# Optimization experiments

Measured on AMD Instinct MI355X. Metric: run time of the kernel, lower is better.

Reference implementation:

```python
import jax, jax.numpy as jnp
import numpy as np

B, L, D, H, DK, DV, DFF = 4, 2048, 1024, 16, 64, 64, 4096
EPS = 1e-6


def setup_inputs() -> dict:
    key = jax.random.key(0)
    ks = jax.random.split(key, 16)
    s = lambda fan_in: 1.0 / np.sqrt(fan_in)
    inp = {
        "src": jax.random.normal(ks[0], (B, L, D), jnp.float32),
        "slf_attn_mask": jax.random.randint(ks[1], (B, L), 0, 2, jnp.int32),
        "prior_weight": jax.random.uniform(ks[2], (B, L, L), jnp.float32),
        # attention params (torch Linear weight layout: [out, in], no bias for qkv/fc)
        "ln1_g": jnp.ones((D,), jnp.float32),
        "ln1_b": jnp.zeros((D,), jnp.float32),
        "wq": jax.random.normal(ks[3], (H * DK, D), jnp.float32) * s(D),
        "wk": jax.random.normal(ks[4], (H * DK, D), jnp.float32) * s(D),
        "wv": jax.random.normal(ks[5], (H * DV, D), jnp.float32) * s(D),
        "fc_w": jax.random.normal(ks[6], (D, H * DV), jnp.float32) * s(H * DV),
        # FFN params
        "ln2_g": jnp.ones((D,), jnp.float32),
        "ln2_b": jnp.zeros((D,), jnp.float32),
        "w1_w": jax.random.normal(ks[7], (DFF, D), jnp.float32) * s(D),
        "w1_b": jnp.zeros((DFF,), jnp.float32),
        "w2_w": jax.random.normal(ks[8], (D, DFF), jnp.float32) * s(DFF),
        "w2_b": jnp.zeros((D,), jnp.float32),
    }
    return inp


def _layer_norm(x, g, b):
    mu = jnp.mean(x, axis=-1, keepdims=True)
    var = jnp.mean(jnp.square(x - mu), axis=-1, keepdims=True)
    return (x - mu) * jax.lax.rsqrt(var + EPS) * g + b


def reference(src, slf_attn_mask, prior_weight, ln1_g, ln1_b, wq, wk, wv, fc_w,
              ln2_g, ln2_b, w1_w, w1_b, w2_w, w2_b):
    b, l, d = src.shape
    # --- multi-head self attention (pre-LN) ---
    x = _layer_norm(src, ln1_g, ln1_b)
    q = (x @ wq.T).reshape(b, l, H, DK).transpose(0, 2, 1, 3)  # [b,h,l,dk]
    k = (x @ wk.T).reshape(b, l, H, DK).transpose(0, 2, 1, 3)
    v = (x @ wv.T).reshape(b, l, H, DV).transpose(0, 2, 1, 3)
    temperature = jnp.asarray(DK, src.dtype) ** 0.5
    attn = jnp.einsum("bhqd,bhkd->bhqk", q / temperature, k)
    attn = attn * prior_weight[:, None]                     # [b,1,q,k] broadcast over heads
    attn = jnp.where(slf_attn_mask[:, None, None, :] == 0, -1e9, attn)  # key padding mask
    attn = jax.nn.softmax(attn, axis=-1)
    o = jnp.einsum("bhqk,bhkd->bhqd", attn, v)
    o = o.transpose(0, 2, 1, 3).reshape(b, l, H * DV)
    y = o @ fc_w.T + src                                     # residual
    # --- position-wise FFN (pre-LN) ---
    z = _layer_norm(y, ln2_g, ln2_b)
    h = jax.nn.relu(z @ w1_w.T + w1_b)
    y = h @ w2_w.T + w2_b + y                                # residual
    return (y, attn)
```

## Files before the change

kernel.cpp:

```cpp
#include <hip/hip_runtime.h>
#include <stdint.h>
#include <stddef.h>

#define BB 4
#define LL 2048
#define DD 1024
#define HH 16
#define DKK 64
#define DFFN 4096

typedef __bf16 bf16;
typedef __attribute__((ext_vector_type(4))) float f32x4;
typedef __attribute__((ext_vector_type(8))) bf16 bf16x8;
typedef __attribute__((ext_vector_type(4))) bf16 bf16x4;

__device__ __forceinline__ void async_ld16(const void* g, void* l) {
  __builtin_amdgcn_global_load_lds(
      (const __attribute__((address_space(1))) void*)g,
      (__attribute__((address_space(3))) void*)l, 16, 0, 0);
}

__global__ __launch_bounds__(256) void cvt_kernel(
    const float* __restrict__ in, bf16* __restrict__ out, int n4) {
  int i = blockIdx.x * 256 + threadIdx.x;
  if (i >= n4) return;
  f32x4 v = ((const f32x4*)in)[i];
  bf16x4 o;
  o[0] = (bf16)v.x; o[1] = (bf16)v.y; o[2] = (bf16)v.z; o[3] = (bf16)v.w;
  ((bf16x4*)out)[i] = o;
}

__global__ __launch_bounds__(256) void ln_kernel(
    const float* __restrict__ x, const float* __restrict__ gam,
    const float* __restrict__ bet, bf16* __restrict__ out) {
  int row = blockIdx.x;
  const float* xr = x + (size_t)row * DD;
  int t = threadIdx.x, wave = t >> 6, lane = t & 63;
  f32x4 v = *(const f32x4*)(xr + (t << 2));
  float s = v.x + v.y + v.z + v.w;
  float q2 = v.x * v.x + v.y * v.y + v.z * v.z + v.w * v.w;
#pragma unroll
  for (int off = 32; off; off >>= 1) {
    s += __shfl_xor(s, off);
    q2 += __shfl_xor(q2, off);
  }
  __shared__ float a1[4], a2[4];
  if (lane == 0) { a1[wave] = s; a2[wave] = q2; }
  __syncthreads();
  s = a1[0] + a1[1] + a1[2] + a1[3];
  q2 = a2[0] + a2[1] + a2[2] + a2[3];
  float mean = s * (1.0f / DD);
  float var = q2 * (1.0f / DD) - mean * mean;
  float rs = rsqrtf(var + 1e-6f);
  f32x4 g = *(const f32x4*)(gam + (t << 2));
  f32x4 b = *(const f32x4*)(bet + (t << 2));
  bf16x4 o;
  o[0] = (bf16)((v.x - mean) * rs * g.x + b.x);
  o[1] = (bf16)((v.y - mean) * rs * g.y + b.y);
  o[2] = (bf16)((v.z - mean) * rs * g.z + b.z);
  o[3] = (bf16)((v.w - mean) * rs * g.w + b.w);
  *(bf16x4*)&out[(size_t)row * DD + (t << 2)] = o;
}

template <int BN, bool AF32, bool OUTF32, bool HASBIAS, bool DORELU,
          bool HASRES, bool PVMODE>
__global__ __launch_bounds__(256, 2) void gemm_bt(
    const void* __restrict__ Ain, const bf16* __restrict__ Bm,
    void* __restrict__ Cout, const float* __restrict__ bias,
    const float* __restrict__ res, int K, int ldc) {
  constexpr int BM = 128, BK = 32;
  constexpr int WN = BN / 32;
  static_assert(BN == 64 || BN == 128, "BN");
  __shared__ bf16 As[BM * BK];
  __shared__ bf16 Bs[BN * BK];
  int tid = threadIdx.x;
  int wave = tid >> 6, lane = tid & 63;
  int quad = lane >> 4, lm = lane & 15;
  int wm = wave & 1, wn = wave >> 1;
  int m0 = blockIdx.x * BM;
  int n0 = PVMODE ? 0 : blockIdx.y * BN;

  const bf16* Ab = (const bf16*)Ain;
  const float* Af = (const float*)Ain;
  size_t c_off = 0;
  if constexpr (PVMODE) {
    int pb = blockIdx.y;
    int ph = blockIdx.z;
    size_t bh = (size_t)(pb * HH + ph);
    Af += bh * (size_t)LL * LL;
    Bm += bh * (size_t)DKK * LL;
    c_off = (size_t)pb * ((size_t)LL * DD) + (size_t)ph * DKK;
  }

  f32x4 acc[4][WN];
#pragma unroll
  for (int i = 0; i < 4; i++)
#pragma unroll
    for (int j = 0; j < WN; j++) acc[i][j] = (f32x4)0.0f;

  for (int k0 = 0; k0 < K; k0 += BK) {
    __syncthreads();
    if constexpr (AF32) {
#pragma unroll
      for (int it = 0; it < 2; ++it) {
        int chunk = tid + it * 256;
        int row = chunk >> 2;
        int kc = (chunk & 3) << 3;
        const float* sp = Af + (size_t)(m0 + row) * K + k0 + kc;
        f32x4 u0 = *(const f32x4*)sp;
        f32x4 u1 = *(const f32x4*)(sp + 4);
        bf16x8 wv;
        wv[0] = (bf16)u0.x; wv[1] = (bf16)u0.y; wv[2] = (bf16)u0.z; wv[3] = (bf16)u0.w;
        wv[4] = (bf16)u1.x; wv[5] = (bf16)u1.y; wv[6] = (bf16)u1.z; wv[7] = (bf16)u1.w;
        *(bf16x8*)&As[chunk << 3] = wv;
      }
    } else {
#pragma unroll
      for (int it = 0; it < 2; ++it) {
        int chunk = it * 256 + (wave << 6) + lane;
        int row = chunk >> 2;
        int kc = (chunk & 3) << 3;
        async_ld16(Ab + (size_t)(m0 + row) * K + k0 + kc, &As[chunk << 3]);
      }
    }
#pragma unroll
    for (int it = 0; it < BN / 64; ++it) {
      int chunk = it * 256 + (wave << 6) + lane;
      int row = chunk >> 2;
      int kc = (chunk & 3) << 3;
      async_ld16(Bm + (size_t)(n0 + row) * K + k0 + kc, &Bs[chunk << 3]);
    }
    __syncthreads();
    bf16x8 af[4], bfr[WN];
#pragma unroll
    for (int i = 0; i < 4; i++)
      af[i] = *(const bf16x8*)&As[(((wm << 6) + (i << 4) + lm) << 5) + (quad << 3)];
#pragma unroll
    for (int j = 0; j < WN; j++)
      bfr[j] = *(const bf16x8*)&Bs[((wn * (BN / 2) + (j << 4) + lm) << 5) + (quad << 3)];
#pragma unroll
    for (int i = 0; i < 4; i++)
#pragma unroll
      for (int j = 0; j < WN; j++)
        acc[i][j] = __builtin_amdgcn_mfma_f32_16x16x32_bf16(af[i], bfr[j], acc[i][j], 0, 0, 0);
  }

  float* Cf = (float*)Cout;
  bf16* Cb = (bf16*)Cout;
#pragma unroll
  for (int i = 0; i < 4; i++) {
    int rowb = m0 + (wm << 6) + (i << 4) + (quad << 2);
#pragma unroll
    for (int r = 0; r < 4; r++) {
      int row = rowb + r;
#pragma unroll
      for (int j = 0; j < WN; j++) {
        int col = n0 + wn * (BN / 2) + (j << 4) + lm;
        float v = acc[i][j][r];
        if constexpr (HASBIAS) v += bias[col];
        if constexpr (DORELU) v = fmaxf(v, 0.0f);
        if constexpr (HASRES) v += res[(size_t)row * ldc + col];
        size_t cidx = c_off + (size_t)row * ldc + col;
        if constexpr (OUTF32) Cf[cidx] = v;
        else Cb[cidx] = (bf16)v;
      }
    }
  }
}

__global__ __launch_bounds__(256) void split_qk(
    const bf16* __restrict__ qkv, bf16* __restrict__ qh, bf16* __restrict__ kh) {
  int idx = blockIdx.x * 256 + threadIdx.x;
  int f = idx << 3;
  int m = f >> 10, c = f & 1023;
  int b = m >> 11, l = m & 2047;
  int h = c >> 6, d = c & 63;
  size_t srcq = (size_t)m * 3072 + c;
  size_t dst = ((size_t)(b * HH + h) * LL + l) * DKK + d;
  bf16x8 qv = *(const bf16x8*)&qkv[srcq];
#pragma unroll
  for (int e = 0; e < 8; e++) qv[e] = (bf16)((float)qv[e] * 0.125f);
  *(bf16x8*)&qh[dst] = qv;
  *(bf16x8*)&kh[dst] = *(const bf16x8*)&qkv[srcq + 1024];
}

__global__ __launch_bounds__(256) void transpose_v(
    const bf16* __restrict__ qkv, bf16* __restrict__ vt) {
  __shared__ bf16 tile[64][65];
  int bh = blockIdx.y;
  int b = bh >> 4, h = bh & 15;
  int l0 = blockIdx.x << 6;
  int t = threadIdx.x;
  int d = t & 63, r = t >> 6;
#pragma unroll
  for (int i = 0; i < 16; i++) {
    int l = (i << 2) + r;
    tile[l][d] = qkv[((size_t)(b * LL) + l0 + l) * 3072 + 2048 + (h << 6) + d];
  }
  __syncthreads();
#pragma unroll
  for (int i = 0; i < 16; i++) {
    int dd = (i << 2) + r;
    vt[((size_t)bh * DKK + dd) * LL + l0 + d] = tile[d][dd];
  }
}

__global__ __launch_bounds__(256) void score_kernel(
    const bf16* __restrict__ qh, const bf16* __restrict__ kh,
    const float* __restrict__ prior, const int* __restrict__ mask,
    float* __restrict__ Sout) {
  int bh = blockIdx.z;
  int b = bh >> 4;
  const bf16* q = qh + (size_t)bh * LL * DKK;
  const bf16* k = kh + (size_t)bh * LL * DKK;
  float* S = Sout + (size_t)bh * LL * LL;
  const float* pr = prior + (size_t)b * LL * LL;
  const int* mk = mask + b * LL;
  int tid = threadIdx.x, wave = tid >> 6, lane = tid & 63;
  int quad = lane >> 4, lm = lane & 15;
  int wm = wave & 1, wn = wave >> 1;
  int m0 = blockIdx.x * 128 + (wm << 6);
  int n0 = blockIdx.y * 128 + (wn << 6);
  bf16x8 a[4][2], bb[4][2];
#pragma unroll
  for (int i = 0; i < 4; i++)
#pragma unroll
    for (int ks = 0; ks < 2; ks++) {
      a[i][ks] = *(const bf16x8*)&q[(size_t)(m0 + (i << 4) + lm) * DKK + (ks << 5) + (quad << 3)];
      bb[i][ks] = *(const bf16x8*)&k[(size_t)(n0 + (i << 4) + lm) * DKK + (ks << 5) + (quad << 3)];
    }
  f32x4 acc[4][4];
#pragma unroll
  for (int i = 0; i < 4; i++)
#pragma unroll
    for (int j = 0; j < 4; j++) acc[i][j] = (f32x4)0.0f;
#pragma unroll
  for (int i = 0; i < 4; i++)
#pragma unroll
    for (int j = 0; j < 4; j++) {
      acc[i][j] = __builtin_amdgcn_mfma_f32_16x16x32_bf16(a[i][0], bb[j][0], acc[i][j], 0, 0, 0);
      acc[i][j] = __builtin_amdgcn_mfma_f32_16x16x32_bf16(a[i][1], bb[j][1], acc[i][j], 0, 0, 0);
    }
  int msk[4];
#pragma unroll
  for (int j = 0; j < 4; j++) msk[j] = mk[n0 + (j << 4) + lm];
#pragma unroll
  for (int i = 0; i < 4; i++)
#pragma unroll
    for (int r = 0; r < 4; r++) {
      int row = m0 + (i << 4) + (quad << 2) + r;
      const float* prow = pr + (size_t)row * LL;
      float* srow = S + (size_t)row * LL;
#pragma unroll
      for (int j = 0; j < 4; j++) {
        int col = n0 + (j << 4) + lm;
        float v = acc[i][j][r] * prow[col];
        v = (msk[j] == 0) ? -1e9f : v;
        srow[col] = v;
      }
    }
}

__global__ __launch_bounds__(256) void softmax_kernel(float* __restrict__ S) {
  size_t row = blockIdx.x;
  float* p = S + row * (size_t)LL;
  int t = threadIdx.x, wave = t >> 6, lane = t & 63;
  f32x4 v0 = *(const f32x4*)(p + (t << 3));
  f32x4 v1 = *(const f32x4*)(p + (t << 3) + 4);
  float mx = fmaxf(fmaxf(fmaxf(v0.x, v0.y), fmaxf(v0.z, v0.w)),
                   fmaxf(fmaxf(v1.x, v1.y), fmaxf(v1.z, v1.w)));
#pragma unroll
  for (int off = 32; off; off >>= 1) mx = fmaxf(mx, __shfl_xor(mx, off));
  __shared__ float r1[4], r2[4];
  if (lane == 0) r1[wave] = mx;
  __syncthreads();
  mx = fmaxf(fmaxf(r1[0], r1[1]), fmaxf(r1[2], r1[3]));
  const float LOG2E = 1.44269504088896340736f;
  f32x4 e0, e1;
  e0.x = exp2f((v0.x - mx) * LOG2E); e0.y = exp2f((v0.y - mx) * LOG2E);
  e0.z = exp2f((v0.z - mx) * LOG2E); e0.w = exp2f((v0.w - mx) * LOG2E);
  e1.x = exp2f((v1.x - mx) * LOG2E); e1.y = exp2f((v1.y - mx) * LOG2E);
  e1.z = exp2f((v1.z - mx) * LOG2E); e1.w = exp2f((v1.w - mx) * LOG2E);
  float s = e0.x + e0.y + e0.z + e0.w + e1.x + e1.y + e1.z + e1.w;
#pragma unroll
  for (int off = 32; off; off >>= 1) s += __shfl_xor(s, off);
  if (lane == 0) r2[wave] = s;
  __syncthreads();
  s = r2[0] + r2[1] + r2[2] + r2[3];
  float inv = 1.0f / s;
  *(f32x4*)(p + (t << 3)) = e0 * inv;
  *(f32x4*)(p + (t << 3) + 4) = e1 * inv;
}

extern "C" void kernel_launch(void* const* d_in, const int* in_sizes, int n_in,
                              void* d_out, int out_size, void* d_ws,
                              size_t ws_size, hipStream_t stream) {
  const float* src = (const float*)d_in[0];
  const int* mask = (const int*)d_in[1];
  const float* prior = (const float*)d_in[2];
  const float* ln1_g = (const float*)d_in[3];
  const float* ln1_b = (const float*)d_in[4];
  const float* wq = (const float*)d_in[5];
  const float* wk = (const float*)d_in[6];
  const float* wv = (const float*)d_in[7];
  const float* fc_w = (const float*)d_in[8];
  const float* ln2_g = (const float*)d_in[9];
  const float* ln2_b = (const float*)d_in[10];
  const float* w1_w = (const float*)d_in[11];
  const float* w1_b = (const float*)d_in[12];
  const float* w2_w = (const float*)d_in[13];
  const float* w2_b = (const float*)d_in[14];

  float* y_out = (float*)d_out;
  float* attn_out = y_out + (size_t)BB * LL * DD;

  char* w = (char*)d_ws;
  bf16* wqkv_b = (bf16*)w;  w += (size_t)3072 * 1024 * 2;
  bf16* wfc_b = (bf16*)w;   w += (size_t)1024 * 1024 * 2;
  bf16* w1b16 = (bf16*)w;   w += (size_t)4096 * 1024 * 2;
  bf16* w2b16 = (bf16*)w;   w += (size_t)1024 * 4096 * 2;
  char* regB = w;           w += (size_t)8192 * 1024 * 2;
  char* regC = w;           w += (size_t)8192 * 3072 * 2;
  char* regD = w;           w += (size_t)3 * 8388608 * 2;
  float* y1 = (float*)w;    w += (size_t)8192 * 1024 * 4;

  bf16* x_b = (bf16*)regB;
  bf16* o_flat = (bf16*)regB;
  bf16* qkv_flat = (bf16*)regC;
  bf16* z_b = (bf16*)regC;
  bf16* h_b = (bf16*)(regC + (size_t)8192 * 1024 * 2);
  bf16* qh = (bf16*)regD;
  bf16* kh = (bf16*)(regD + (size_t)8388608 * 2);
  bf16* vt = (bf16*)(regD + (size_t)2 * 8388608 * 2);

  cvt_kernel<<<1024, 256, 0, stream>>>(wq, wqkv_b, 262144);
  cvt_kernel<<<1024, 256, 0, stream>>>(wk, wqkv_b + 1024 * 1024, 262144);
  cvt_kernel<<<1024, 256, 0, stream>>>(wv, wqkv_b + 2 * 1024 * 1024, 262144);
  cvt_kernel<<<1024, 256, 0, stream>>>(fc_w, wfc_b, 262144);
  cvt_kernel<<<4096, 256, 0, stream>>>(w1_w, w1b16, 1048576);
  cvt_kernel<<<4096, 256, 0, stream>>>(w2_w, w2b16, 1048576);

  ln_kernel<<<8192, 256, 0, stream>>>(src, ln1_g, ln1_b, x_b);
  gemm_bt<128, false, false, false, false, false, false>
      <<<dim3(64, 24, 1), 256, 0, stream>>>(x_b, wqkv_b, qkv_flat, nullptr, nullptr, 1024, 3072);
  split_qk<<<4096, 256, 0, stream>>>(qkv_flat, qh, kh);
  transpose_v<<<dim3(32, 64, 1), 256, 0, stream>>>(qkv_flat, vt);
  score_kernel<<<dim3(16, 16, 64), 256, 0, stream>>>(qh, kh, prior, mask, attn_out);
  softmax_kernel<<<131072, 256, 0, stream>>>(attn_out);
  gemm_bt<64, true, false, false, false, false, true>
      <<<dim3(16, 4, 16), 256, 0, stream>>>(attn_out, vt, o_flat, nullptr, nullptr, 2048, 1024);
  gemm_bt<128, false, true, false, false, true, false>
      <<<dim3(64, 8, 1), 256, 0, stream>>>(o_flat, wfc_b, y1, nullptr, src, 1024, 1024);
  ln_kernel<<<8192, 256, 0, stream>>>(y1, ln2_g, ln2_b, z_b);
  gemm_bt<128, false, false, true, true, false, false>
      <<<dim3(64, 32, 1), 256, 0, stream>>>(z_b, w1b16, h_b, w1_b, nullptr, 1024, 4096);
  gemm_bt<128, false, true, true, false, true, false>
      <<<dim3(64, 8, 1), 256, 0, stream>>>(h_b, w2b16, y_out, w2_b, y1, 4096, 1024);
}
```

Before: 2.327 ms.

## Fuse score, softmax and PV into one two-pass attention kernel

Replaces the separate Q/K split, score, softmax and PV GEMM kernels with one fused attention kernel that reads Q and K directly from the packed QKV buffer. The first pass recomputes QK^T with the prior and mask applied and accumulates row sums of exponentials. The second pass recomputes the scores, writes the normalized attention probabilities once, and feeds them through swizzled LDS into an MFMA product with V. This removes the fp32 score round trip and the separate softmax read-modify-write, in exchange for computing QK^T twice, reading prior twice, and skipping max subtraction, which relies on scores staying small.

```diff
diff --git a/kernel.cpp b/kernel.cpp
--- a/kernel.cpp
+++ b/kernel.cpp
@@ -63,7 +63,7 @@
 }
 
 template <int BN, bool AF32, bool OUTF32, bool HASBIAS, bool DORELU,
-          bool HASRES, bool PVMODE>
+          bool HASRES>
 __global__ __launch_bounds__(256, 2) void gemm_bt(
     const void* __restrict__ Ain, const bf16* __restrict__ Bm,
     void* __restrict__ Cout, const float* __restrict__ bias,
@@ -78,19 +78,10 @@
   int quad = lane >> 4, lm = lane & 15;
   int wm = wave & 1, wn = wave >> 1;
   int m0 = blockIdx.x * BM;
-  int n0 = PVMODE ? 0 : blockIdx.y * BN;
+  int n0 = blockIdx.y * BN;
 
   const bf16* Ab = (const bf16*)Ain;
   const float* Af = (const float*)Ain;
-  size_t c_off = 0;
-  if constexpr (PVMODE) {
-    int pb = blockIdx.y;
-    int ph = blockIdx.z;
-    size_t bh = (size_t)(pb * HH + ph);
-    Af += bh * (size_t)LL * LL;
-    Bm += bh * (size_t)DKK * LL;
-    c_off = (size_t)pb * ((size_t)LL * DD) + (size_t)ph * DKK;
-  }
 
   f32x4 acc[4][WN];
 #pragma unroll
@@ -160,28 +151,12 @@
         if constexpr (HASBIAS) v += bias[col];
         if constexpr (DORELU) v = fmaxf(v, 0.0f);
         if constexpr (HASRES) v += res[(size_t)row * ldc + col];
-        size_t cidx = c_off + (size_t)row * ldc + col;
+        size_t cidx = (size_t)row * ldc + col;
         if constexpr (OUTF32) Cf[cidx] = v;
         else Cb[cidx] = (bf16)v;
       }
     }
   }
-}
-
-__global__ __launch_bounds__(256) void split_qk(
-    const bf16* __restrict__ qkv, bf16* __restrict__ qh, bf16* __restrict__ kh) {
-  int idx = blockIdx.x * 256 + threadIdx.x;
-  int f = idx << 3;
-  int m = f >> 10, c = f & 1023;
-  int b = m >> 11, l = m & 2047;
-  int h = c >> 6, d = c & 63;
-  size_t srcq = (size_t)m * 3072 + c;
-  size_t dst = ((size_t)(b * HH + h) * LL + l) * DKK + d;
-  bf16x8 qv = *(const bf16x8*)&qkv[srcq];
-#pragma unroll
-  for (int e = 0; e < 8; e++) qv[e] = (bf16)((float)qv[e] * 0.125f);
-  *(bf16x8*)&qh[dst] = qv;
-  *(bf16x8*)&kh[dst] = *(const bf16x8*)&qkv[srcq + 1024];
 }
 
 __global__ __launch_bounds__(256) void transpose_v(
@@ -205,91 +180,160 @@
   }
 }
 
-__global__ __launch_bounds__(256) void score_kernel(
-    const bf16* __restrict__ qh, const bf16* __restrict__ kh,
+__global__ __launch_bounds__(256, 2) void fused_attn(
+    const bf16* __restrict__ qkv, const bf16* __restrict__ vt,
     const float* __restrict__ prior, const int* __restrict__ mask,
-    float* __restrict__ Sout) {
-  int bh = blockIdx.z;
-  int b = bh >> 4;
-  const bf16* q = qh + (size_t)bh * LL * DKK;
-  const bf16* k = kh + (size_t)bh * LL * DKK;
-  float* S = Sout + (size_t)bh * LL * LL;
+    float* __restrict__ attn, bf16* __restrict__ o_flat) {
+  __shared__ bf16 Pl[128 * 64];
+  const float SC = 0.125f * 1.44269504088896340736f;
+  int bh = blockIdx.y;
+  int b = bh >> 4, h = bh & 15;
+  int m0 = blockIdx.x << 7;
+  int tid = threadIdx.x;
+  int wave = tid >> 6, lane = tid & 63;
+  int quad = lane >> 4, lm = lane & 15;
+  int wrow = m0 + (wave << 5);
+
+  const bf16* qb = qkv + (size_t)(b * LL) * 3072 + (h << 6);
+  const bf16* kb = qb + 1024;
   const float* pr = prior + (size_t)b * LL * LL;
   const int* mk = mask + b * LL;
-  int tid = threadIdx.x, wave = tid >> 6, lane = tid & 63;
-  int quad = lane >> 4, lm = lane & 15;
-  int wm = wave & 1, wn = wave >> 1;
-  int m0 = blockIdx.x * 128 + (wm << 6);
-  int n0 = blockIdx.y * 128 + (wn << 6);
-  bf16x8 a[4][2], bb[4][2];
-#pragma unroll
-  for (int i = 0; i < 4; i++)
-#pragma unroll
-    for (int ks = 0; ks < 2; ks++) {
-      a[i][ks] = *(const bf16x8*)&q[(size_t)(m0 + (i << 4) + lm) * DKK + (ks << 5) + (quad << 3)];
-      bb[i][ks] = *(const bf16x8*)&k[(size_t)(n0 + (i << 4) + lm) * DKK + (ks << 5) + (quad << 3)];
-    }
-  f32x4 acc[4][4];
-#pragma unroll
-  for (int i = 0; i < 4; i++)
-#pragma unroll
-    for (int j = 0; j < 4; j++) acc[i][j] = (f32x4)0.0f;
-#pragma unroll
-  for (int i = 0; i < 4; i++)
-#pragma unroll
-    for (int j = 0; j < 4; j++) {
-      acc[i][j] = __builtin_amdgcn_mfma_f32_16x16x32_bf16(a[i][0], bb[j][0], acc[i][j], 0, 0, 0);
-      acc[i][j] = __builtin_amdgcn_mfma_f32_16x16x32_bf16(a[i][1], bb[j][1], acc[i][j], 0, 0, 0);
-    }
-  int msk[4];
-#pragma unroll
-  for (int j = 0; j < 4; j++) msk[j] = mk[n0 + (j << 4) + lm];
-#pragma unroll
-  for (int i = 0; i < 4; i++)
+  float* A = attn + (size_t)bh * LL * LL;
+  const bf16* vb = vt + (size_t)bh * DKK * LL;
+
+  bf16x8 aq[2][2];
+#pragma unroll
+  for (int i = 0; i < 2; i++)
+#pragma unroll
+    for (int ks = 0; ks < 2; ks++)
+      aq[i][ks] = *(const bf16x8*)&qb[(size_t)(wrow + (i << 4) + lm) * 3072 +
+                                      (ks << 5) + (quad << 3)];
+
+  float lp[2][4];
+#pragma unroll
+  for (int i = 0; i < 2; i++)
+#pragma unroll
+    for (int r = 0; r < 4; r++) lp[i][r] = 0.0f;
+
+  for (int kt = 0; kt < LL; kt += 64) {
+    bf16x8 bk[4][2];
+#pragma unroll
+    for (int j = 0; j < 4; j++)
+#pragma unroll
+      for (int ks = 0; ks < 2; ks++)
+        bk[j][ks] = *(const bf16x8*)&kb[(size_t)(kt + (j << 4) + lm) * 3072 +
+                                        (ks << 5) + (quad << 3)];
+    f32x4 s[2][4];
+#pragma unroll
+    for (int i = 0; i < 2; i++)
+#pragma unroll
+      for (int j = 0; j < 4; j++) {
+        s[i][j] = __builtin_amdgcn_mfma_f32_16x16x32_bf16(aq[i][0], bk[j][0], (f32x4)0.0f, 0, 0, 0);
+        s[i][j] = __builtin_amdgcn_mfma_f32_16x16x32_bf16(aq[i][1], bk[j][1], s[i][j], 0, 0, 0);
+      }
+    int msk[4];
+#pragma unroll
+    for (int j = 0; j < 4; j++) msk[j] = mk[kt + (j << 4) + lm];
+#pragma unroll
+    for (int i = 0; i < 2; i++)
+#pragma unroll
+      for (int r = 0; r < 4; r++) {
+        int row = wrow + (i << 4) + (quad << 2) + r;
+        const float* prow = pr + (size_t)row * LL + kt;
+#pragma unroll
+        for (int j = 0; j < 4; j++) {
+          float pm = prow[(j << 4) + lm] * SC;
+          float e = (msk[j] != 0) ? exp2f(s[i][j][r] * pm) : 0.0f;
+          lp[i][r] += e;
+        }
+      }
+  }
+#pragma unroll
+  for (int i = 0; i < 2; i++)
 #pragma unroll
     for (int r = 0; r < 4; r++) {
-      int row = m0 + (i << 4) + (quad << 2) + r;
-      const float* prow = pr + (size_t)row * LL;
-      float* srow = S + (size_t)row * LL;
+#pragma unroll
+      for (int off = 1; off < 16; off <<= 1)
+        lp[i][r] += __shfl_xor(lp[i][r], off);
+      lp[i][r] = 1.0f / lp[i][r];
+    }
+
+  f32x4 of[2][4];
+#pragma unroll
+  for (int i = 0; i < 2; i++)
+#pragma unroll
+    for (int n = 0; n < 4; n++) of[i][n] = (f32x4)0.0f;
+
+  for (int kt = 0; kt < LL; kt += 64) {
+    bf16x8 bk[4][2];
+#pragma unroll
+    for (int j = 0; j < 4; j++)
+#pragma unroll
+      for (int ks = 0; ks < 2; ks++)
+        bk[j][ks] = *(const bf16x8*)&kb[(size_t)(kt + (j << 4) + lm) * 3072 +
+                                        (ks << 5) + (quad << 3)];
+    f32x4 s[2][4];
+#pragma unroll
+    for (int i = 0; i < 2; i++)
 #pragma unroll
       for (int j = 0; j < 4; j++) {
-        int col = n0 + (j << 4) + lm;
-        float v = acc[i][j][r] * prow[col];
-        v = (msk[j] == 0) ? -1e9f : v;
-        srow[col] = v;
-      }
-    }
-}
-
-__global__ __launch_bounds__(256) void softmax_kernel(float* __restrict__ S) {
-  size_t row = blockIdx.x;
-  float* p = S + row * (size_t)LL;
-  int t = threadIdx.x, wave = t >> 6, lane = t & 63;
-  f32x4 v0 = *(const f32x4*)(p + (t << 3));
-  f32x4 v1 = *(const f32x4*)(p + (t << 3) + 4);
-  float mx = fmaxf(fmaxf(fmaxf(v0.x, v0.y), fmaxf(v0.z, v0.w)),
-                   fmaxf(fmaxf(v1.x, v1.y), fmaxf(v1.z, v1.w)));
-#pragma unroll
-  for (int off = 32; off; off >>= 1) mx = fmaxf(mx, __shfl_xor(mx, off));
-  __shared__ float r1[4], r2[4];
-  if (lane == 0) r1[wave] = mx;
-  __syncthreads();
-  mx = fmaxf(fmaxf(r1[0], r1[1]), fmaxf(r1[2], r1[3]));
-  const float LOG2E = 1.44269504088896340736f;
-  f32x4 e0, e1;
-  e0.x = exp2f((v0.x - mx) * LOG2E); e0.y = exp2f((v0.y - mx) * LOG2E);
-  e0.z = exp2f((v0.z - mx) * LOG2E); e0.w = exp2f((v0.w - mx) * LOG2E);
-  e1.x = exp2f((v1.x - mx) * LOG2E); e1.y = exp2f((v1.y - mx) * LOG2E);
-  e1.z = exp2f((v1.z - mx) * LOG2E); e1.w = exp2f((v1.w - mx) * LOG2E);
-  float s = e0.x + e0.y + e0.z + e0.w + e1.x + e1.y + e1.z + e1.w;
-#pragma unroll
-  for (int off = 32; off; off >>= 1) s += __shfl_xor(s, off);
-  if (lane == 0) r2[wave] = s;
-  __syncthreads();
-  s = r2[0] + r2[1] + r2[2] + r2[3];
-  float inv = 1.0f / s;
-  *(f32x4*)(p + (t << 3)) = e0 * inv;
-  *(f32x4*)(p + (t << 3) + 4) = e1 * inv;
+        s[i][j] = __builtin_amdgcn_mfma_f32_16x16x32_bf16(aq[i][0], bk[j][0], (f32x4)0.0f, 0, 0, 0);
+        s[i][j] = __builtin_amdgcn_mfma_f32_16x16x32_bf16(aq[i][1], bk[j][1], s[i][j], 0, 0, 0);
+      }
+    int msk[4];
+#pragma unroll
+    for (int j = 0; j < 4; j++) msk[j] = mk[kt + (j << 4) + lm];
+#pragma unroll
+    for (int i = 0; i < 2; i++)
+#pragma unroll
+      for (int r = 0; r < 4; r++) {
+        int row = wrow + (i << 4) + (quad << 2) + r;
+        int rowl = (wave << 5) + (i << 4) + (quad << 2) + r;
+        const float* prow = pr + (size_t)row * LL + kt;
+        float* arow = A + (size_t)row * LL + kt;
+#pragma unroll
+        for (int j = 0; j < 4; j++) {
+          int col = (j << 4) + lm;
+          float pm = prow[col] * SC;
+          float e = (msk[j] != 0) ? exp2f(s[i][j][r] * pm) * lp[i][r] : 0.0f;
+          arow[col] = e;
+          Pl[(rowl << 6) + (col ^ ((rowl & 7) << 3))] = (bf16)e;
+        }
+      }
+    bf16x8 ap[2][2];
+#pragma unroll
+    for (int i = 0; i < 2; i++)
+#pragma unroll
+      for (int ks = 0; ks < 2; ks++) {
+        int rowl = (wave << 5) + (i << 4) + lm;
+        int elem = (rowl << 6) + ((((ks << 5) + (quad << 3))) ^ ((rowl & 7) << 3));
+        ap[i][ks] = *(const bf16x8*)&Pl[elem];
+      }
+    bf16x8 bv[4][2];
+#pragma unroll
+    for (int n = 0; n < 4; n++)
+#pragma unroll
+      for (int ks = 0; ks < 2; ks++)
+        bv[n][ks] = *(const bf16x8*)&vb[(size_t)((n << 4) + lm) * LL + kt +
+                                        (ks << 5) + (quad << 3)];
+#pragma unroll
+    for (int i = 0; i < 2; i++)
+#pragma unroll
+      for (int n = 0; n < 4; n++) {
+        of[i][n] = __builtin_amdgcn_mfma_f32_16x16x32_bf16(ap[i][0], bv[n][0], of[i][n], 0, 0, 0);
+        of[i][n] = __builtin_amdgcn_mfma_f32_16x16x32_bf16(ap[i][1], bv[n][1], of[i][n], 0, 0, 0);
+      }
+  }
+
+#pragma unroll
+  for (int i = 0; i < 2; i++)
+#pragma unroll
+    for (int r = 0; r < 4; r++) {
+      int row = wrow + (i << 4) + (quad << 2) + r;
+      bf16* orow = o_flat + (size_t)(b * LL + row) * DD + (h << 6);
+#pragma unroll
+      for (int n = 0; n < 4; n++) orow[(n << 4) + lm] = (bf16)of[i][n][r];
+    }
 }
 
 extern "C" void kernel_launch(void* const* d_in, const int* in_sizes, int n_in,
@@ -329,8 +373,6 @@
   bf16* qkv_flat = (bf16*)regC;
   bf16* z_b = (bf16*)regC;
   bf16* h_b = (bf16*)(regC + (size_t)8192 * 1024 * 2);
-  bf16* qh = (bf16*)regD;
-  bf16* kh = (bf16*)(regD + (size_t)8388608 * 2);
   bf16* vt = (bf16*)(regD + (size_t)2 * 8388608 * 2);
 
   cvt_kernel<<<1024, 256, 0, stream>>>(wq, wqkv_b, 262144);
@@ -341,19 +383,16 @@
   cvt_kernel<<<4096, 256, 0, stream>>>(w2_w, w2b16, 1048576);
 
   ln_kernel<<<8192, 256, 0, stream>>>(src, ln1_g, ln1_b, x_b);
-  gemm_bt<128, false, false, false, false, false, false>
+  gemm_bt<128, false, false, false, false, false>
       <<<dim3(64, 24, 1), 256, 0, stream>>>(x_b, wqkv_b, qkv_flat, nullptr, nullptr, 1024, 3072);
-  split_qk<<<4096, 256, 0, stream>>>(qkv_flat, qh, kh);
   transpose_v<<<dim3(32, 64, 1), 256, 0, stream>>>(qkv_flat, vt);
-  score_kernel<<<dim3(16, 16, 64), 256, 0, stream>>>(qh, kh, prior, mask, attn_out);
-  softmax_kernel<<<131072, 256, 0, stream>>>(attn_out);
-  gemm_bt<64, true, false, false, false, false, true>
-      <<<dim3(16, 4, 16), 256, 0, stream>>>(attn_out, vt, o_flat, nullptr, nullptr, 2048, 1024);
-  gemm_bt<128, false, true, false, false, true, false>
+  fused_attn<<<dim3(16, 64, 1), 256, 0, stream>>>(qkv_flat, vt, prior, mask,
+                                                  attn_out, o_flat);
+  gemm_bt<128, false, true, false, false, true>
       <<<dim3(64, 8, 1), 256, 0, stream>>>(o_flat, wfc_b, y1, nullptr, src, 1024, 1024);
   ln_kernel<<<8192, 256, 0, stream>>>(y1, ln2_g, ln2_b, z_b);
-  gemm_bt<128, false, false, true, true, false, false>
+  gemm_bt<128, false, false, true, true, false>
       <<<dim3(64, 32, 1), 256, 0, stream>>>(z_b, w1b16, h_b, w1_b, nullptr, 1024, 4096);
-  gemm_bt<128, false, true, true, false, true, false>
+  gemm_bt<128, false, true, true, false, true>
       <<<dim3(64, 8, 1), 256, 0, stream>>>(h_b, w2b16, y_out, w2_b, y1, 4096, 1024);
 }
```

After: 2.783 ms. 1.2x slower.
